# Optimization experiments

Measured on AMD Instinct MI355X. Metric: run time of the kernel, lower is better.

## Reference

```python
import jax, jax.numpy as jnp
import numpy as np

D_MODEL = 1024
NUM_HEADS = 16
HEAD_DIM = D_MODEL // NUM_HEADS


def setup_inputs() -> dict:
    key = jax.random.key(0)
    ks = jax.random.split(key, 11)
    B, S = 4, 2048
    s = 1.0 / np.sqrt(D_MODEL)
    inp = {
        "query": jax.random.normal(ks[0], (B, S, D_MODEL), jnp.float32),
        "key": jax.random.normal(ks[1], (B, S, D_MODEL), jnp.float32),
        "value": jax.random.normal(ks[2], (B, S, D_MODEL), jnp.float32),
        "Wq": jax.random.normal(ks[3], (D_MODEL, D_MODEL), jnp.float32) * s,
        "bq": jnp.zeros((D_MODEL,), jnp.float32),
        "Wk": jax.random.normal(ks[4], (D_MODEL, D_MODEL), jnp.float32) * s,
        "bk": jnp.zeros((D_MODEL,), jnp.float32),
        "Wv": jax.random.normal(ks[5], (D_MODEL, D_MODEL), jnp.float32) * s,
        "bv": jnp.zeros((D_MODEL,), jnp.float32),
        "Wo": jax.random.normal(ks[6], (D_MODEL, D_MODEL), jnp.float32) * s,
        "bo": jnp.zeros((D_MODEL,), jnp.float32),
    }
    return inp


def reference(query, key, value, Wq, bq, Wk, bk, Wv, bv, Wo, bo):
    B, S, _ = query.shape
    def proj(x, W, b):  # [B,S,D] -> [B,H,S,hd]
        y = jnp.einsum("bsd,ed->bse", x, W) + b
        return y.reshape(B, -1, NUM_HEADS, HEAD_DIM).transpose(0, 2, 1, 3)
    q = proj(query, Wq, bq)
    k = proj(key, Wk, bk)
    v = proj(value, Wv, bv)
    scores = jnp.einsum("bhqd,bhkd->bhqk", q, k) / np.sqrt(HEAD_DIM).astype(jnp.float32)
    attn = jax.nn.softmax(scores, axis=-1)
    out = jnp.einsum("bhqk,bhkd->bhqd", attn, v)
    out = out.transpose(0, 2, 1, 3).reshape(B, -1, D_MODEL)
    return jnp.einsum("bsd,ed->bse", out, Wo) + bo
```

## Files before the change

### kernel.cpp

```cpp
#include <hip/hip_runtime.h>
#include <math.h>

#define DM    1024
#define NH    16
#define HD    64
#define SEQ   2048
#define BATCH 4
#define TOKENS (BATCH * SEQ)

typedef _Float16 half2v __attribute__((ext_vector_type(2)));
typedef __fp16   fp16x2 __attribute__((ext_vector_type(2)));
typedef _Float16 half4  __attribute__((ext_vector_type(4)));
typedef _Float16 half8  __attribute__((ext_vector_type(8)));
typedef float    f32x4  __attribute__((ext_vector_type(4)));

typedef const __attribute__((address_space(1))) void* gas_p;
typedef __attribute__((address_space(3))) void*       las_p;

__device__ __forceinline__ void gload_lds16(const void* g, void* l) {
    __builtin_amdgcn_global_load_lds((gas_p)g, (las_p)l, 16, 0, 0);
}

__device__ __forceinline__ half2v pack2(float a, float b) {
    fp16x2 r = __builtin_amdgcn_cvt_pkrtz(a, b);
    return __builtin_bit_cast(half2v, r);
}

#define MFMA16(a, b, c) __builtin_amdgcn_mfma_f32_16x16x32_f16((a), (b), (c), 0, 0, 0)

__global__ __launch_bounds__(256) void cvt_all(
    const float* __restrict__ q, const float* __restrict__ k,
    const float* __restrict__ v, const float* __restrict__ wq,
    const float* __restrict__ wk, const float* __restrict__ wv,
    const float* __restrict__ wo, _Float16* __restrict__ dst)
{
    const size_t TD = (size_t)TOKENS * DM, WD = (size_t)DM * DM;
    const size_t i = ((size_t)blockIdx.x * 256 + threadIdx.x) * 4;
    const float* s; size_t off;
    if      (i <     TD)          { s = q;  off = i; }
    else if (i < 2 * TD)          { s = k;  off = i - TD; }
    else if (i < 3 * TD)          { s = v;  off = i - 2 * TD; }
    else if (i < 3 * TD + WD)     { s = wq; off = i - 3 * TD; }
    else if (i < 3 * TD + 2 * WD) { s = wk; off = i - 3 * TD - WD; }
    else if (i < 3 * TD + 3 * WD) { s = wv; off = i - 3 * TD - 2 * WD; }
    else                          { s = wo; off = i - 3 * TD - 3 * WD; }
    const float4 x = *(const float4*)(s + off);
    half4 h = { (_Float16)x.x, (_Float16)x.y, (_Float16)x.z, (_Float16)x.w };
    *(half4*)(dst + i) = h;
}

__global__ __launch_bounds__(256) void qkv_gemm(
    const _Float16* __restrict__ Abase, const _Float16* __restrict__ Wbase,
    const float* __restrict__ bq, const float* __restrict__ bk,
    const float* __restrict__ bv, _Float16* __restrict__ Cbase, float qscale)
{
    __shared__ __align__(16) _Float16 As[128 * 32];
    __shared__ __align__(16) _Float16 Ws[128 * 32];

    const int z = blockIdx.z;
    const size_t TD = (size_t)TOKENS * DM, WD = (size_t)DM * DM;
    const _Float16* A = Abase + (size_t)z * TD;
    const _Float16* W = Wbase + (size_t)z * WD;
    const float* bias = (z == 0) ? bq : (z == 1) ? bk : bv;
    _Float16* C = Cbase + (size_t)z * TD;
    const float scale = (z == 0) ? qscale : 1.0f;

    const int t = threadIdx.x;
    const int w = t >> 6, l = t & 63;
    const int tx = l & 15, quad = l >> 4;
    const int m0 = blockIdx.x * 128, n0 = blockIdx.y * 128;
    const int wm = (w & 1) * 64, wn = (w >> 1) * 64;
    const int srow = t >> 2, schk = t & 3;

    const _Float16* Ag = A + (size_t)m0 * DM;
    const _Float16* Wg = W + (size_t)n0 * DM;

    f32x4 acc[4][4] = {};

    for (int k0 = 0; k0 < DM; k0 += 32) {
        __syncthreads();
        #pragma unroll
        for (int i = 0; i < 2; ++i) {
            gload_lds16(Ag + (size_t)(i * 64 + srow) * DM + k0 + schk * 8,
                        As + (size_t)(i * 256 + (t & ~63)) * 8);
            gload_lds16(Wg + (size_t)(i * 64 + srow) * DM + k0 + schk * 8,
                        Ws + (size_t)(i * 256 + (t & ~63)) * 8);
        }
        __syncthreads();

        half8 af[4], bf[4];
        #pragma unroll
        for (int mt = 0; mt < 4; ++mt)
            af[mt] = *(const half8*)(As + (wm + mt * 16 + tx) * 32 + quad * 8);
        #pragma unroll
        for (int nt = 0; nt < 4; ++nt)
            bf[nt] = *(const half8*)(Ws + (wn + nt * 16 + tx) * 32 + quad * 8);
        #pragma unroll
        for (int mt = 0; mt < 4; ++mt)
            #pragma unroll
            for (int nt = 0; nt < 4; ++nt)
                acc[mt][nt] = MFMA16(af[mt], bf[nt], acc[mt][nt]);
    }

    float bsv[4];
    #pragma unroll
    for (int nt = 0; nt < 4; ++nt) bsv[nt] = bias[n0 + wn + nt * 16 + tx];

    #pragma unroll
    for (int mt = 0; mt < 4; ++mt) {
        #pragma unroll
        for (int nt = 0; nt < 4; ++nt) {
            const int n = n0 + wn + nt * 16 + tx;
            const int mr0 = m0 + wm + mt * 16 + quad * 4;
            const int h = n >> 6, d = n & 63;
            if (z < 2) {
                #pragma unroll
                for (int r = 0; r < 4; ++r) {
                    const int m = mr0 + r;
                    const int b = m >> 11, s = m & (SEQ - 1);
                    const float vv = (acc[mt][nt][r] + bsv[nt]) * scale;
                    C[(((size_t)b * NH + h) * SEQ + s) * HD + d] = (_Float16)vv;
                }
            } else {
                const int b = mr0 >> 11, s0 = mr0 & (SEQ - 1);
                half4 hv = { (_Float16)(acc[mt][nt][0] + bsv[nt]),
                             (_Float16)(acc[mt][nt][1] + bsv[nt]),
                             (_Float16)(acc[mt][nt][2] + bsv[nt]),
                             (_Float16)(acc[mt][nt][3] + bsv[nt]) };
                *(half4*)(C + (((size_t)b * NH + h) * HD + d) * SEQ + s0) = hv;
            }
        }
    }
}

__global__ __launch_bounds__(256) void out_gemm(
    const _Float16* __restrict__ A, const _Float16* __restrict__ W,
    const float* __restrict__ bias, float* __restrict__ C)
{
    __shared__ __align__(16) _Float16 As[128 * 32];
    __shared__ __align__(16) _Float16 Ws[128 * 32];

    const int t = threadIdx.x;
    const int w = t >> 6, l = t & 63;
    const int tx = l & 15, quad = l >> 4;
    const int m0 = blockIdx.x * 128, n0 = blockIdx.y * 128;
    const int wm = (w & 1) * 64, wn = (w >> 1) * 64;
    const int srow = t >> 2, schk = t & 3;

    const _Float16* Ag = A + (size_t)m0 * DM;
    const _Float16* Wg = W + (size_t)n0 * DM;

    f32x4 acc[4][4] = {};

    for (int k0 = 0; k0 < DM; k0 += 32) {
        __syncthreads();
        #pragma unroll
        for (int i = 0; i < 2; ++i) {
            gload_lds16(Ag + (size_t)(i * 64 + srow) * DM + k0 + schk * 8,
                        As + (size_t)(i * 256 + (t & ~63)) * 8);
            gload_lds16(Wg + (size_t)(i * 64 + srow) * DM + k0 + schk * 8,
                        Ws + (size_t)(i * 256 + (t & ~63)) * 8);
        }
        __syncthreads();

        half8 af[4], bf[4];
        #pragma unroll
        for (int mt = 0; mt < 4; ++mt)
            af[mt] = *(const half8*)(As + (wm + mt * 16 + tx) * 32 + quad * 8);
        #pragma unroll
        for (int nt = 0; nt < 4; ++nt)
            bf[nt] = *(const half8*)(Ws + (wn + nt * 16 + tx) * 32 + quad * 8);
        #pragma unroll
        for (int mt = 0; mt < 4; ++mt)
            #pragma unroll
            for (int nt = 0; nt < 4; ++nt)
                acc[mt][nt] = MFMA16(af[mt], bf[nt], acc[mt][nt]);
    }

    float bsv[4];
    #pragma unroll
    for (int nt = 0; nt < 4; ++nt) bsv[nt] = bias[n0 + wn + nt * 16 + tx];

    #pragma unroll
    for (int mt = 0; mt < 4; ++mt)
        #pragma unroll
        for (int nt = 0; nt < 4; ++nt) {
            const int n = n0 + wn + nt * 16 + tx;
            const int mr0 = m0 + wm + mt * 16 + quad * 4;
            #pragma unroll
            for (int r = 0; r < 4; ++r)
                C[(size_t)(mr0 + r) * DM + n] = acc[mt][nt][r] + bsv[nt];
        }
}

__global__ __launch_bounds__(256, 3) void flash16(
    const _Float16* __restrict__ Q, const _Float16* __restrict__ K,
    const _Float16* __restrict__ Vt, _Float16* __restrict__ AO)
{
    __shared__ __align__(16) char pool[51200];
    __shared__ float lW[128];

    const int t = threadIdx.x, w = t >> 6, l = t & 63;
    const int tx = l & 15, quad = l >> 4;
    const int q0 = blockIdx.x * 128;
    const int bh = blockIdx.y, b = bh >> 4, h = bh & 15;

    const _Float16* Qg = Q + ((size_t)bh * SEQ + q0 + w * 32) * HD;
    const _Float16* Kg = K + (size_t)bh * SEQ * HD;
    const _Float16* Vg = Vt + (size_t)bh * HD * SEQ;
    _Float16* Pw = (_Float16*)(pool + 32768 + w * 4608);

    const int srow = l >> 3;
    const int schk = (l & 7) ^ (srow & 7);

    half8 Qf[2][2];
    #pragma unroll
    for (int ks = 0; ks < 2; ++ks)
        #pragma unroll
        for (int qt = 0; qt < 2; ++qt)
            Qf[ks][qt] = *(const half8*)(Qg + (size_t)(qt * 16 + tx) * HD + ks * 32 + quad * 8);

    f32x4 Oa[2][4] = {};
    float l2[2] = {0.f, 0.f};
    const half2v one2 = { (_Float16)1.0f, (_Float16)1.0f };

    {
        _Float16* KL = (_Float16*)(pool);
        _Float16* VL = (_Float16*)(pool + 16384);
        #pragma unroll
        for (int jj = 0; jj < 2; ++jj) {
            const int j = w + jj * 4;
            const int row = 8 * j + srow;
            gload_lds16(Kg + (size_t)row * HD + schk * 8, KL + j * 512);
            gload_lds16(Vg + (size_t)row * SEQ + schk * 8, VL + j * 512);
        }
    }

    for (int it = 0; it < SEQ / 64; ++it) {
        __syncthreads();

        if (it < SEQ / 64 - 1) {
            const int kb = (it + 1) * 64;
            _Float16* KL = (_Float16*)(pool + ((it + 1) & 1) * 8192);
            _Float16* VL = (_Float16*)(pool + 16384 + ((it + 1) & 1) * 8192);
            #pragma unroll
            for (int jj = 0; jj < 2; ++jj) {
                const int j = w + jj * 4;
                const int row = 8 * j + srow;
                gload_lds16(Kg + (size_t)(kb + row) * HD + schk * 8, KL + j * 512);
                gload_lds16(Vg + (size_t)row * SEQ + kb + schk * 8, VL + j * 512);
            }
        }

        const _Float16* KL = (const _Float16*)(pool + (it & 1) * 8192);
        const _Float16* VL = (const _Float16*)(pool + 16384 + (it & 1) * 8192);

        half8 kf[4][2];
        #pragma unroll
        for (int kt = 0; kt < 4; ++kt)
            #pragma unroll
            for (int ks = 0; ks < 2; ++ks)
                kf[kt][ks] = *(const half8*)(KL + (kt * 16 + tx) * 64 +
                                             (((ks * 4 + quad) ^ (tx & 7)) * 8));

        f32x4 sa[2][4];
        #pragma unroll
        for (int qt = 0; qt < 2; ++qt)
            #pragma unroll
            for (int kt = 0; kt < 4; ++kt) {
                f32x4 s = {0.f, 0.f, 0.f, 0.f};
                s = MFMA16(kf[kt][0], Qf[0][qt], s);
                s = MFMA16(kf[kt][1], Qf[1][qt], s);
                sa[qt][kt] = s;
            }

        half8 vf[4][2];
        #pragma unroll
        for (int dt = 0; dt < 4; ++dt)
            #pragma unroll
            for (int kst = 0; kst < 2; ++kst)
                vf[dt][kst] = *(const half8*)(VL + (dt * 16 + tx) * 64 +
                                              (((kst * 4 + quad) ^ (tx & 7)) * 8));

        #pragma unroll
        for (int qt = 0; qt < 2; ++qt)
            #pragma unroll
            for (int kt = 0; kt < 4; ++kt) {
                const float p0 = __builtin_amdgcn_exp2f(sa[qt][kt][0]);
                const float p1 = __builtin_amdgcn_exp2f(sa[qt][kt][1]);
                const float p2 = __builtin_amdgcn_exp2f(sa[qt][kt][2]);
                const float p3 = __builtin_amdgcn_exp2f(sa[qt][kt][3]);
                const half2v pa = pack2(p0, p1);
                const half2v pb = pack2(p2, p3);
                l2[qt] = __builtin_amdgcn_fdot2(pa, one2, l2[qt], false);
                l2[qt] = __builtin_amdgcn_fdot2(pb, one2, l2[qt], false);
                half4 pk = { pa.x, pa.y, pb.x, pb.y };
                *(half4*)(Pw + (qt * 16 + tx) * 72 + kt * 16 + quad * 4) = pk;
            }

        half8 pf[2][2];
        #pragma unroll
        for (int qt = 0; qt < 2; ++qt)
            #pragma unroll
            for (int kst = 0; kst < 2; ++kst)
                pf[qt][kst] = *(const half8*)(Pw + (qt * 16 + tx) * 72 + kst * 32 + quad * 8);
        #pragma unroll
        for (int qt = 0; qt < 2; ++qt)
            #pragma unroll
            for (int dt = 0; dt < 4; ++dt) {
                Oa[qt][dt] = MFMA16(pf[qt][0], vf[dt][0], Oa[qt][dt]);
                Oa[qt][dt] = MFMA16(pf[qt][1], vf[dt][1], Oa[qt][dt]);
            }
    }

    #pragma unroll
    for (int qt = 0; qt < 2; ++qt) {
        l2[qt] += __shfl_xor(l2[qt], 16, 64);
        l2[qt] += __shfl_xor(l2[qt], 32, 64);
    }
    if (quad == 0) {
        #pragma unroll
        for (int qt = 0; qt < 2; ++qt) lW[w * 32 + qt * 16 + tx] = l2[qt];
    }
    __syncthreads();

    float* Ob = (float*)pool;
    #pragma unroll
    for (int qt = 0; qt < 2; ++qt)
        #pragma unroll
        for (int dt = 0; dt < 4; ++dt)
            #pragma unroll
            for (int r = 0; r < 4; ++r)
                Ob[(w * 32 + qt * 16 + quad * 4 + r) * 68 + dt * 16 + tx] = Oa[qt][dt][r];
    __syncthreads();

    {
        const int row = t >> 1, cb = (t & 1) * 32;
        const float inv = 1.0f / lW[row];
        _Float16* dst = AO + ((size_t)b * SEQ + q0 + row) * DM + h * HD + cb;
        #pragma unroll
        for (int j = 0; j < 32; j += 8) {
            const f32x4 o0 = *(const f32x4*)(Ob + row * 68 + cb + j);
            const f32x4 o1 = *(const f32x4*)(Ob + row * 68 + cb + j + 4);
            half8 hv = { (_Float16)(o0[0] * inv), (_Float16)(o0[1] * inv),
                         (_Float16)(o0[2] * inv), (_Float16)(o0[3] * inv),
                         (_Float16)(o1[0] * inv), (_Float16)(o1[1] * inv),
                         (_Float16)(o1[2] * inv), (_Float16)(o1[3] * inv) };
            *(half8*)(dst + j) = hv;
        }
    }
}

extern "C" void kernel_launch(void* const* d_in, const int* in_sizes, int n_in,
                              void* d_out, int out_size, void* d_ws, size_t ws_size,
                              hipStream_t stream)
{
    const float* q  = (const float*)d_in[0];
    const float* k  = (const float*)d_in[1];
    const float* v  = (const float*)d_in[2];
    const float* Wq = (const float*)d_in[3];
    const float* bq = (const float*)d_in[4];
    const float* Wk = (const float*)d_in[5];
    const float* bk = (const float*)d_in[6];
    const float* Wv = (const float*)d_in[7];
    const float* bv = (const float*)d_in[8];
    const float* Wo = (const float*)d_in[9];
    const float* bo = (const float*)d_in[10];
    float* out = (float*)d_out;

    const size_t TD = (size_t)TOKENS * DM;
    const size_t WD = (size_t)DM * DM;
    _Float16* ws = (_Float16*)d_ws;
    _Float16* cvtbase = ws;
    _Float16* q16  = ws;
    _Float16* wq16 = ws + 3 * TD;
    _Float16* wo16 = wq16 + 3 * WD;
    _Float16* Qw   = ws + 3 * TD + 4 * WD;
    _Float16* Kw   = Qw + TD;
    _Float16* Vtw  = Kw + TD;
    _Float16* AOw  = Vtw + TD;

    const int gC = (int)((3 * TD + 4 * WD) / 4 / 256);
    cvt_all<<<gC, 256, 0, stream>>>(q, k, v, Wq, Wk, Wv, Wo, cvtbase);

    const float qscale = 0.18033688011112042f;
    qkv_gemm<<<dim3(TOKENS / 128, DM / 128, 3), 256, 0, stream>>>(
        q16, wq16, bq, bk, bv, Qw, qscale);

    flash16<<<dim3(SEQ / 128, BATCH * NH, 1), 256, 0, stream>>>(Qw, Kw, Vtw, AOw);

    out_gemm<<<dim3(TOKENS / 128, DM / 128, 1), 256, 0, stream>>>(AOw, wo16, bo, out);
}
```

Measured before the change: 373.3 us.

## Switch flash attention to 32x32 MFMA with register-resident P via permlane swap

Rewrites the attention inner loop to use 32x32x16 MFMA tiles instead of 16x16x32. The S accumulator layout now lets P be fed straight into the PV MFMA through permlane32_swap, removing the LDS write and read round-trip for P and shrinking shared memory. It also remaps the 1-D grid so each head's query blocks land on the same XCD for L2 reuse of K/V, and adds s_setprio around the MFMA phases. The risks are higher register pressure from the f32x16 accumulators and correctness depending on the permlane layout matching the MFMA operand layout.

Measured after the change: 340.4 us. 1.1x faster.

```diff
diff --git a/kernel.cpp b/kernel.cpp
--- a/kernel.cpp
+++ b/kernel.cpp
@@ -13,6 +13,9 @@
 typedef _Float16 half4  __attribute__((ext_vector_type(4)));
 typedef _Float16 half8  __attribute__((ext_vector_type(8)));
 typedef float    f32x4  __attribute__((ext_vector_type(4)));
+typedef float    f32x16 __attribute__((ext_vector_type(16)));
+typedef unsigned int u32x2 __attribute__((ext_vector_type(2)));
+typedef unsigned int u32x4 __attribute__((ext_vector_type(4)));
 
 typedef const __attribute__((address_space(1))) void* gas_p;
 typedef __attribute__((address_space(3))) void*       las_p;
@@ -21,12 +24,13 @@
     __builtin_amdgcn_global_load_lds((gas_p)g, (las_p)l, 16, 0, 0);
 }
 
-__device__ __forceinline__ half2v pack2(float a, float b) {
+__device__ __forceinline__ unsigned pack2u(float a, float b) {
     fp16x2 r = __builtin_amdgcn_cvt_pkrtz(a, b);
-    return __builtin_bit_cast(half2v, r);
+    return __builtin_bit_cast(unsigned, r);
 }
 
 #define MFMA16(a, b, c) __builtin_amdgcn_mfma_f32_16x16x32_f16((a), (b), (c), 0, 0, 0)
+#define MFMA32(a, b, c) __builtin_amdgcn_mfma_f32_32x32x16_f16((a), (b), (c), 0, 0, 0)
 
 __global__ __launch_bounds__(256) void cvt_all(
     const float* __restrict__ q, const float* __restrict__ k,
@@ -197,31 +201,32 @@
     const _Float16* __restrict__ Q, const _Float16* __restrict__ K,
     const _Float16* __restrict__ Vt, _Float16* __restrict__ AO)
 {
-    __shared__ __align__(16) char pool[51200];
+    __shared__ __align__(16) char pool[34816];
     __shared__ float lW[128];
 
     const int t = threadIdx.x, w = t >> 6, l = t & 63;
-    const int tx = l & 15, quad = l >> 4;
-    const int q0 = blockIdx.x * 128;
-    const int bh = blockIdx.y, b = bh >> 4, h = bh & 15;
+    const int lid = l & 31, hl = l >> 5;
+
+    const int bid = blockIdx.x;
+    const int xcd = bid & 7, loc = bid >> 3;
+    const int bh = xcd * 8 + (loc >> 4);
+    const int q0 = (loc & 15) * 128;
+    const int b = bh >> 4, h = bh & 15;
 
     const _Float16* Qg = Q + ((size_t)bh * SEQ + q0 + w * 32) * HD;
     const _Float16* Kg = K + (size_t)bh * SEQ * HD;
     const _Float16* Vg = Vt + (size_t)bh * HD * SEQ;
-    _Float16* Pw = (_Float16*)(pool + 32768 + w * 4608);
 
     const int srow = l >> 3;
-    const int schk = (l & 7) ^ (srow & 7);
-
-    half8 Qf[2][2];
-    #pragma unroll
-    for (int ks = 0; ks < 2; ++ks)
-        #pragma unroll
-        for (int qt = 0; qt < 2; ++qt)
-            Qf[ks][qt] = *(const half8*)(Qg + (size_t)(qt * 16 + tx) * HD + ks * 32 + quad * 8);
-
-    f32x4 Oa[2][4] = {};
-    float l2[2] = {0.f, 0.f};
+    const int schk = (l & 7) ^ srow;
+
+    half8 Qf[4];
+    #pragma unroll
+    for (int ks = 0; ks < 4; ++ks)
+        Qf[ks] = *(const half8*)(Qg + (size_t)lid * HD + ks * 16 + hl * 8);
+
+    f32x16 Oa[2] = {};
+    float l2 = 0.f;
     const half2v one2 = { (_Float16)1.0f, (_Float16)1.0f };
 
     {
@@ -255,83 +260,80 @@
         const _Float16* KL = (const _Float16*)(pool + (it & 1) * 8192);
         const _Float16* VL = (const _Float16*)(pool + 16384 + (it & 1) * 8192);
 
-        half8 kf[4][2];
-        #pragma unroll
-        for (int kt = 0; kt < 4; ++kt)
-            #pragma unroll
-            for (int ks = 0; ks < 2; ++ks)
-                kf[kt][ks] = *(const half8*)(KL + (kt * 16 + tx) * 64 +
-                                             (((ks * 4 + quad) ^ (tx & 7)) * 8));
-
-        f32x4 sa[2][4];
-        #pragma unroll
-        for (int qt = 0; qt < 2; ++qt)
-            #pragma unroll
-            for (int kt = 0; kt < 4; ++kt) {
-                f32x4 s = {0.f, 0.f, 0.f, 0.f};
-                s = MFMA16(kf[kt][0], Qf[0][qt], s);
-                s = MFMA16(kf[kt][1], Qf[1][qt], s);
-                sa[qt][kt] = s;
+        half8 kf[2][4];
+        #pragma unroll
+        for (int kt = 0; kt < 2; ++kt)
+            #pragma unroll
+            for (int ks = 0; ks < 4; ++ks)
+                kf[kt][ks] = *(const half8*)(KL + (kt * 32 + lid) * 64 +
+                                             (((ks * 2 + hl) ^ (lid & 7)) * 8));
+
+        f32x16 sacc[2];
+        __builtin_amdgcn_s_setprio(1);
+        #pragma unroll
+        for (int kt = 0; kt < 2; ++kt) {
+            f32x16 s = {};
+            #pragma unroll
+            for (int ks = 0; ks < 4; ++ks)
+                s = MFMA32(kf[kt][ks], Qf[ks], s);
+            sacc[kt] = s;
+        }
+        __builtin_amdgcn_s_setprio(0);
+
+        half8 vf[4][2];
+        #pragma unroll
+        for (int kstep = 0; kstep < 4; ++kstep)
+            #pragma unroll
+            for (int dt = 0; dt < 2; ++dt)
+                vf[kstep][dt] = *(const half8*)(VL + (dt * 32 + lid) * 64 +
+                                                (((kstep * 2 + hl) ^ (lid & 7)) * 8));
+
+        unsigned cf[2][4][2];
+        #pragma unroll
+        for (int kt = 0; kt < 2; ++kt)
+            #pragma unroll
+            for (int g = 0; g < 4; ++g) {
+                const float p0 = __builtin_amdgcn_exp2f(sacc[kt][g * 4 + 0]);
+                const float p1 = __builtin_amdgcn_exp2f(sacc[kt][g * 4 + 1]);
+                const float p2 = __builtin_amdgcn_exp2f(sacc[kt][g * 4 + 2]);
+                const float p3 = __builtin_amdgcn_exp2f(sacc[kt][g * 4 + 3]);
+                const unsigned ca = pack2u(p0, p1);
+                const unsigned cb = pack2u(p2, p3);
+                l2 = __builtin_amdgcn_fdot2(__builtin_bit_cast(half2v, ca), one2, l2, false);
+                l2 = __builtin_amdgcn_fdot2(__builtin_bit_cast(half2v, cb), one2, l2, false);
+                cf[kt][g][0] = ca;
+                cf[kt][g][1] = cb;
             }
 
-        half8 vf[4][2];
-        #pragma unroll
-        for (int dt = 0; dt < 4; ++dt)
-            #pragma unroll
-            for (int kst = 0; kst < 2; ++kst)
-                vf[dt][kst] = *(const half8*)(VL + (dt * 16 + tx) * 64 +
-                                              (((kst * 4 + quad) ^ (tx & 7)) * 8));
-
-        #pragma unroll
-        for (int qt = 0; qt < 2; ++qt)
-            #pragma unroll
-            for (int kt = 0; kt < 4; ++kt) {
-                const float p0 = __builtin_amdgcn_exp2f(sa[qt][kt][0]);
-                const float p1 = __builtin_amdgcn_exp2f(sa[qt][kt][1]);
-                const float p2 = __builtin_amdgcn_exp2f(sa[qt][kt][2]);
-                const float p3 = __builtin_amdgcn_exp2f(sa[qt][kt][3]);
-                const half2v pa = pack2(p0, p1);
-                const half2v pb = pack2(p2, p3);
-                l2[qt] = __builtin_amdgcn_fdot2(pa, one2, l2[qt], false);
-                l2[qt] = __builtin_amdgcn_fdot2(pb, one2, l2[qt], false);
-                half4 pk = { pa.x, pa.y, pb.x, pb.y };
-                *(half4*)(Pw + (qt * 16 + tx) * 72 + kt * 16 + quad * 4) = pk;
-            }
-
-        half8 pf[2][2];
-        #pragma unroll
-        for (int qt = 0; qt < 2; ++qt)
-            #pragma unroll
-            for (int kst = 0; kst < 2; ++kst)
-                pf[qt][kst] = *(const half8*)(Pw + (qt * 16 + tx) * 72 + kst * 32 + quad * 8);
-        #pragma unroll
-        for (int qt = 0; qt < 2; ++qt)
-            #pragma unroll
-            for (int dt = 0; dt < 4; ++dt) {
-                Oa[qt][dt] = MFMA16(pf[qt][0], vf[dt][0], Oa[qt][dt]);
-                Oa[qt][dt] = MFMA16(pf[qt][1], vf[dt][1], Oa[qt][dt]);
-            }
-    }
-
-    #pragma unroll
-    for (int qt = 0; qt < 2; ++qt) {
-        l2[qt] += __shfl_xor(l2[qt], 16, 64);
-        l2[qt] += __shfl_xor(l2[qt], 32, 64);
-    }
-    if (quad == 0) {
-        #pragma unroll
-        for (int qt = 0; qt < 2; ++qt) lW[w * 32 + qt * 16 + tx] = l2[qt];
-    }
+        __builtin_amdgcn_s_setprio(1);
+        #pragma unroll
+        for (int kstep = 0; kstep < 4; ++kstep) {
+            const int kt = kstep >> 1, g0 = (kstep & 1) * 2;
+            const u32x2 r0 = __builtin_amdgcn_permlane32_swap(
+                cf[kt][g0][0], cf[kt][g0 + 1][0], false, false);
+            const u32x2 r1 = __builtin_amdgcn_permlane32_swap(
+                cf[kt][g0][1], cf[kt][g0 + 1][1], false, false);
+            const u32x4 pw = { r0[0], r1[0], r0[1], r1[1] };
+            const half8 pa = __builtin_bit_cast(half8, pw);
+            #pragma unroll
+            for (int dt = 0; dt < 2; ++dt)
+                Oa[dt] = MFMA32(pa, vf[kstep][dt], Oa[dt]);
+        }
+        __builtin_amdgcn_s_setprio(0);
+    }
+
+    l2 += __shfl_xor(l2, 32, 64);
+    if (l < 32) lW[w * 32 + l] = l2;
     __syncthreads();
 
     float* Ob = (float*)pool;
     #pragma unroll
-    for (int qt = 0; qt < 2; ++qt)
-        #pragma unroll
-        for (int dt = 0; dt < 4; ++dt)
+    for (int dt = 0; dt < 2; ++dt)
+        #pragma unroll
+        for (int g = 0; g < 4; ++g)
             #pragma unroll
             for (int r = 0; r < 4; ++r)
-                Ob[(w * 32 + qt * 16 + quad * 4 + r) * 68 + dt * 16 + tx] = Oa[qt][dt][r];
+                Ob[(w * 32 + g * 8 + hl * 4 + r) * 68 + dt * 32 + lid] = Oa[dt][g * 4 + r];
     __syncthreads();
 
     {
@@ -387,7 +389,7 @@
     qkv_gemm<<<dim3(TOKENS / 128, DM / 128, 3), 256, 0, stream>>>(
         q16, wq16, bq, bk, bv, Qw, qscale);
 
-    flash16<<<dim3(SEQ / 128, BATCH * NH, 1), 256, 0, stream>>>(Qw, Kw, Vtw, AOw);
+    flash16<<<dim3((SEQ / 128) * BATCH * NH), 256, 0, stream>>>(Qw, Kw, Vtw, AOw);
 
     out_gemm<<<dim3(TOKENS / 128, DM / 128, 1), 256, 0, stream>>>(AOw, wo16, bo, out);
 }
```
